# Kernel tuning notes

Hardware: AMD Instinct MI355X
Metric: run time of the kernel (lower is better)

Reference implementation:

```python
import jax, jax.numpy as jnp
import numpy as np

# --- HashGrid constants (from init_kwargs) ---
L = 16                 # num_lods
T = 1 << 18            # hashmap entries per level (codebook_bitwidth=18)
F = 2                  # feature_dim per level
BASE = 16              # min_width_codebook
MAXW = 1 << 12         # max_width_codebook
SCALE = np.exp((np.log(MAXW) - np.log(BASE)) / L)
RES = np.floor(BASE * SCALE ** np.arange(L)).astype(np.float32)  # per-level grid resolution
P1 = np.uint32(2654435761)  # coherent-prime hash primes (prime for x is 1)
P2 = np.uint32(805459861)
OFFS = np.array([[i, j, k] for i in (0, 1) for j in (0, 1) for k in (0, 1)], np.int32)  # [8,3] cube corners


def _hash_encode(x, tables):
    """x: [N,3] in [0,1]. tables: [L,T,F]. Returns [N, 3 + L*F] (include_xyz)."""
    def level(table, res):
        xs = x * res                              # [N,3] scaled coords
        x0 = jnp.floor(xs)
        t = xs - x0                               # fractional part
        w = t * t * (3.0 - 2.0 * t)               # Smoothstep interpolation weights
        c = x0.astype(jnp.int32)[:, None, :] + OFFS[None]    # [N,8,3] corner coords
        cu = c.astype(jnp.uint32)
        h = (cu[..., 0] ^ (cu[..., 1] * P1) ^ (cu[..., 2] * P2)) & jnp.uint32(T - 1)  # [N,8]
        feats = table[h]                          # [N,8,F] irregular gather
        wts = jnp.prod(jnp.where(OFFS[None] == 1, w[:, None, :], 1.0 - w[:, None, :]), axis=-1)  # [N,8]
        return jnp.einsum('ncf,nc->nf', feats, wts)  # [N,F]

    f = jax.vmap(level)(tables, jnp.asarray(RES))   # [L,N,F]
    f = jnp.moveaxis(f, 0, 1).reshape(x.shape[0], L * F)
    return jnp.concatenate([x, f], axis=-1)         # include_xyz prepends raw coords


def setup_inputs() -> dict:
    key = jax.random.key(0)
    k1, k2, k3, k4 = jax.random.split(key, 4)
    N = 1 << 20
    x = jax.random.uniform(k1, (N, 3), dtype=jnp.float32)
    tables = jax.random.normal(k2, (L, T, F), dtype=jnp.float32) * 1e-2
    d_in = 3 + L * F    # 35
    W1 = jax.random.normal(k3, (d_in, 128), dtype=jnp.float32) / np.sqrt(d_in)
    W2 = jax.random.normal(k4, (128, 129), dtype=jnp.float32) / np.sqrt(128.0)
    return {"x": x, "tables": tables, "W1": W1, "W2": W2}


def reference(x, tables, W1, W2):
    enc = _hash_encode(x, tables)        # [N,35]
    h = jax.nn.relu(enc @ W1)            # VanillaMLP: one hidden layer, bias-free
    return h @ W2                        # [N, 1+geo_feat_dim], Identity output act
```

## Files before the change

### kernel.cpp

```cpp
#include <hip/hip_runtime.h>

typedef __attribute__((ext_vector_type(8))) short short8;
typedef __attribute__((ext_vector_type(4))) float f32x4;
typedef __attribute__((ext_vector_type(4))) int int4v;

#define TMASK  ((1u << 18) - 1u)
#define PRIME1 2654435761u
#define PRIME2 805459861u

__constant__ float c_res[16] = {16.f, 22.f, 31.f, 45.f, 63.f, 90.f, 127.f, 181.f,
                                255.f, 362.f, 511.f, 724.f, 1023.f, 1448.f, 2047.f, 2896.f};

__device__ __forceinline__ unsigned short rne_bf16(float v) {
  unsigned u = __builtin_bit_cast(unsigned, v);
  return (unsigned short)((u + 0x7fffu + ((u >> 16) & 1u)) >> 16);
}
__device__ __forceinline__ float b2f(unsigned short h) {
  unsigned u = (unsigned)h << 16;
  return __builtin_bit_cast(float, u);
}

__device__ __forceinline__ float2 enc_level(float x0, float x1, float x2, int lvl,
                                            const float* __restrict__ Tb) {
  const float r = c_res[lvl];
  const float xs0 = x0 * r, xs1 = x1 * r, xs2 = x2 * r;
  const float f0 = floorf(xs0), f1 = floorf(xs1), f2 = floorf(xs2);
  const float t0 = xs0 - f0, t1 = xs1 - f1, t2 = xs2 - f2;
  const float w0 = t0 * t0 * (3.f - 2.f * t0);
  const float w1v = t1 * t1 * (3.f - 2.f * t1);
  const float w2v = t2 * t2 * (3.f - 2.f * t2);
  const unsigned cx0 = (unsigned)(int)f0;
  const unsigned hy0 = (unsigned)(int)f1 * PRIME1, hy1 = hy0 + PRIME1;
  const unsigned hz0 = (unsigned)(int)f2 * PRIME2, hz1 = hz0 + PRIME2;
  const float2* tab = reinterpret_cast<const float2*>(Tb) + ((size_t)lvl << 18);
  float a0 = 0.f, a1 = 0.f;
  if (!(cx0 & 1u)) {
    const float4* tab4 = reinterpret_cast<const float4*>(tab);
#pragma unroll
    for (int jk = 0; jk < 4; ++jk) {
      const unsigned hb = (cx0 ^ ((jk & 2) ? hy1 : hy0) ^ ((jk & 1) ? hz1 : hz0)) & TMASK;
      const float4 q = tab4[hb >> 1];
      float e0x, e0y, e1x, e1y;
      if (hb & 1) { e0x = q.z; e0y = q.w; e1x = q.x; e1y = q.y; }
      else        { e0x = q.x; e0y = q.y; e1x = q.z; e1y = q.w; }
      const float wy = (jk & 2) ? w1v : 1.f - w1v;
      const float wz = (jk & 1) ? w2v : 1.f - w2v;
      const float wt0 = ((1.f - w0) * wy) * wz;
      const float wt1 = (w0 * wy) * wz;
      a0 = fmaf(e0x, wt0, a0); a1 = fmaf(e0y, wt0, a1);
      a0 = fmaf(e1x, wt1, a0); a1 = fmaf(e1y, wt1, a1);
    }
  } else {
#pragma unroll
    for (int c = 0; c < 8; ++c) {
      const unsigned hx = cx0 + (unsigned)((c >> 2) & 1);
      const unsigned hh = (hx ^ ((c & 2) ? hy1 : hy0) ^ ((c & 1) ? hz1 : hz0)) & TMASK;
      const float2 f = tab[hh];
      const float wt = (((c >> 2) & 1) ? w0 : 1.f - w0) *
                       (((c >> 1) & 1) ? w1v : 1.f - w1v) *
                       (((c & 1)) ? w2v : 1.f - w2v);
      a0 = fmaf(f.x, wt, a0);
      a1 = fmaf(f.y, wt, a1);
    }
  }
  return make_float2(a0, a1);
}

__global__ __launch_bounds__(256, 2) void fused_pc(
    const float* __restrict__ X, const float* __restrict__ Tb,
    const float* __restrict__ W1, const float* __restrict__ W2,
    unsigned short* __restrict__ encF, int* __restrict__ flags,
    float* __restrict__ Out) {
  __shared__ __align__(16) unsigned char lds[76800];
  __shared__ int ldsflag;
  unsigned short* w1S  = (unsigned short*)lds;
  float*          w1x  = (float*)(lds + 8192);
  float*          xyzS = (float*)(lds + 9728);
  unsigned short* w2hS = (unsigned short*)(lds + 10752);
  float*          hS   = (float*)(lds + 43776);
  float*          outS = (float*)(lds + 43776);

  const int tid = threadIdx.x;
  const int lane = tid & 63, w = tid >> 6;
  const int b = blockIdx.x;
  const int g = b & 7;
  const int bslot = b >> 3;
  const int lvlA = g, lvlB = 15 - g;

  for (int idx = tid; idx < 32 * 128; idx += 256) {
    const int k = idx >> 7, col = idx & 127;
    w1S[((k >> 3) * 128 + col) * 8 + (k & 7)] = rne_bf16(W1[(k + 3) * 128 + col]);
  }
  for (int idx = tid; idx < 3 * 128; idx += 256) w1x[idx] = W1[idx];
  for (int idx = tid; idx < 128 * 129; idx += 256) {
    const int k = idx / 129, col = idx - k * 129;
    w2hS[((k >> 3) * 129 + col) * 8 + (k & 7)] = rne_bf16(W2[idx]);
  }
  __syncthreads();

  int nextI = 0;

  auto mlp_chunk = [&](int chunk) {
    const size_t base_int = ((size_t)(chunk * 4 + w) * 64 + lane) * 4;
    int4v ai;
#pragma unroll
    for (int e = 0; e < 4; ++e)
      ai[e] = __hip_atomic_load((int*)encF + base_int + e,
                                __ATOMIC_RELAXED, __HIP_MEMORY_SCOPE_SYSTEM);
    const short8 af = __builtin_bit_cast(short8, ai);
    const int row0 = chunk << 6;
    if (tid < 192) xyzS[(tid / 3) * 4 + (tid % 3)] = X[(size_t)row0 * 3 + tid];
    __syncthreads();

    f32x4 acc1[8];
#pragma unroll
    for (int c = 0; c < 8; ++c) acc1[c] = (f32x4){0.f, 0.f, 0.f, 0.f};
#pragma unroll
    for (int c = 0; c < 8; ++c) {
      const short8 bb = *reinterpret_cast<const short8*>(
          &w1S[((lane >> 4) * 128 + c * 16 + (lane & 15)) * 8]);
      acc1[c] = __builtin_amdgcn_mfma_f32_16x16x32_bf16(af, bb, acc1[c], 0, 0, 0);
    }
#pragma unroll
    for (int r = 0; r < 4; ++r) {
      const int grow = (w << 4) + (lane >> 4) * 4 + r;
      const float xs0 = xyzS[grow * 4 + 0];
      const float xs1 = xyzS[grow * 4 + 1];
      const float xs2 = xyzS[grow * 4 + 2];
#pragma unroll
      for (int c = 0; c < 8; ++c) {
        const int col = c * 16 + (lane & 15);
        float v = acc1[c][r];
        v = fmaf(xs0, w1x[col], v);
        v = fmaf(xs1, w1x[128 + col], v);
        v = fmaf(xs2, w1x[256 + col], v);
        acc1[c][r] = v;
      }
    }
#pragma unroll
    for (int c = 0; c < 8; ++c) {
#pragma unroll
      for (int r = 0; r < 4; ++r) {
        const int row = (w << 4) + (lane >> 4) * 4 + r;
        const int col = c * 16 + (lane & 15);
        const int cc = (col >> 2) ^ (row & 7);
        hS[row * 128 + (cc << 2) + (col & 3)] = fmaxf(acc1[c][r], 0.f);
      }
    }
    __syncthreads();

    const int arow = (w << 4) + (lane & 15);
    short8 a2h[4], a2l[4];
#pragma unroll
    for (int kc = 0; kc < 4; ++kc) {
      const int c8 = kc * 4 + (lane >> 4);
      const int base = arow * 128;
      const int cc0 = (2 * c8) ^ (arow & 7);
      const int cc1 = (2 * c8 + 1) ^ (arow & 7);
      const f32x4 q0 = *reinterpret_cast<const f32x4*>(&hS[base + (cc0 << 2)]);
      const f32x4 q1 = *reinterpret_cast<const f32x4*>(&hS[base + (cc1 << 2)]);
#pragma unroll
      for (int e = 0; e < 4; ++e) {
        const unsigned short hi = rne_bf16(q0[e]);
        a2h[kc][e] = (short)hi;
        a2l[kc][e] = (short)rne_bf16(q0[e] - b2f(hi));
      }
#pragma unroll
      for (int e = 0; e < 4; ++e) {
        const unsigned short hi = rne_bf16(q1[e]);
        a2h[kc][4 + e] = (short)hi;
        a2l[kc][4 + e] = (short)rne_bf16(q1[e] - b2f(hi));
      }
    }
    __syncthreads();

#pragma unroll
    for (int c = 0; c < 9; ++c) {
      f32x4 acc = (f32x4){0.f, 0.f, 0.f, 0.f};
      int bcol = c * 16 + (lane & 15);
      if (bcol > 128) bcol = 128;
#pragma unroll
      for (int kc = 0; kc < 4; ++kc) {
        const int c8 = kc * 4 + (lane >> 4);
        const short8 bh = *reinterpret_cast<const short8*>(&w2hS[(c8 * 129 + bcol) * 8]);
        acc = __builtin_amdgcn_mfma_f32_16x16x32_bf16(a2h[kc], bh, acc, 0, 0, 0);
        acc = __builtin_amdgcn_mfma_f32_16x16x32_bf16(a2l[kc], bh, acc, 0, 0, 0);
      }
      const int col = c * 16 + (lane & 15);
      if (col < 129) {
#pragma unroll
        for (int r = 0; r < 4; ++r) {
          const int lrow = (w << 4) + (lane >> 4) * 4 + r;
          outS[lrow * 129 + col] = acc[r];
        }
      }
    }
    __syncthreads();

    float* dst = Out + (size_t)row0 * 129;
    const f32x4* src = (const f32x4*)outS;
    for (int i = tid; i < 2064; i += 256)
      __builtin_nontemporal_store(src[i], reinterpret_cast<f32x4*>(dst + 4 * i));
  };

  for (int t = 0; t < 64; ++t) {
    const int grp = bslot + t * 64;
    {
      const int p = (grp << 8) + tid;
      const float x0 = X[p * 3 + 0];
      const float x1 = X[p * 3 + 1];
      const float x2 = X[p * 3 + 2];
      const int pl = p & 63, chunk = p >> 6;
      const size_t rowbase = ((size_t)(chunk * 4 + (pl >> 4)) * 64 + (pl & 15)) * 8;
#pragma unroll
      for (int li = 0; li < 2; ++li) {
        const int lvl = li ? lvlB : lvlA;
        const float2 a = enc_level(x0, x1, x2, lvl, Tb);
        const int c8 = lvl >> 2;
        const size_t addr_short = rowbase + (size_t)(c8 << 7) + (lvl & 3) * 2;
        const int val = (int)rne_bf16(a.x) | ((int)rne_bf16(a.y) << 16);
        __hip_atomic_store((int*)encF + (addr_short >> 1), val,
                           __ATOMIC_RELAXED, __HIP_MEMORY_SCOPE_SYSTEM);
      }
    }
    __syncthreads();
    if (tid == 0)
      __hip_atomic_fetch_add(&flags[grp], 1, __ATOMIC_RELAXED, __HIP_MEMORY_SCOPE_SYSTEM);

    while (nextI < 32) {
      const int c = b + (nextI << 9);
      if (tid == 0)
        ldsflag = __hip_atomic_load(&flags[c >> 2], __ATOMIC_RELAXED,
                                    __HIP_MEMORY_SCOPE_SYSTEM);
      __syncthreads();
      if (ldsflag != 8) break;
      mlp_chunk(c);
      ++nextI;
    }
  }

  while (nextI < 32) {
    const int c = b + (nextI << 9);
    for (;;) {
      if (tid == 0)
        ldsflag = __hip_atomic_load(&flags[c >> 2], __ATOMIC_RELAXED,
                                    __HIP_MEMORY_SCOPE_SYSTEM);
      __syncthreads();
      if (ldsflag == 8) break;
      __builtin_amdgcn_s_sleep(32);
      __syncthreads();
    }
    mlp_chunk(c);
    ++nextI;
  }
}

__global__ __launch_bounds__(256) void fused_hashmlp(
    const float* __restrict__ X, const float* __restrict__ Tb,
    const float* __restrict__ W1, const float* __restrict__ W2,
    float* __restrict__ Out, int nChunks) {
  __shared__ __align__(16) unsigned char lds[147968];
  unsigned short* w1hS = (unsigned short*)lds;
  unsigned short* w1lS = w1hS + 128 * 64;
  unsigned short* w2hS = (unsigned short*)(lds + 32768);
  unsigned short* w2lS = w2hS + 129 * 128;
  unsigned short* enchS = (unsigned short*)(lds + 98816);
  unsigned short* enclS = enchS + 64 * 64;
  float*          hS    = (float*)(lds + 115200);
  float*          outS  = (float*)(lds + 98816);

  const int tid = threadIdx.x;
  for (int idx = tid; idx < 128 * 64; idx += 256) {
    int k = idx >> 7, col = idx & 127;
    float v = 0.f;
    if (k < 35) { int r = (k < 32) ? (k + 3) : (k - 32); v = W1[r * 128 + col]; }
    unsigned short hi = rne_bf16(v);
    unsigned short lo = rne_bf16(v - b2f(hi));
    int a = col * 64 + (k ^ ((col & 7) << 3));
    w1hS[a] = hi; w1lS[a] = lo;
  }
  for (int idx = tid; idx < 129 * 128; idx += 256) {
    int k = idx / 129, col = idx - k * 129;
    float v = W2[k * 129 + col];
    unsigned short hi = rne_bf16(v);
    unsigned short lo = rne_bf16(v - b2f(hi));
    int a = col * 128 + (k ^ ((col & 7) << 3));
    w2hS[a] = hi; w2lS[a] = lo;
  }
  __syncthreads();

  const int p = tid >> 2, s = tid & 3, lane = tid & 63, w = tid >> 6;
  for (int chunk = blockIdx.x; chunk < nChunks; chunk += gridDim.x) {
    const int row0 = chunk * 64;
    {
      const int gp = row0 + p;
      const float x0 = X[gp * 3 + 0], x1 = X[gp * 3 + 1], x2 = X[gp * 3 + 2];
      short8 pkh, pkl;
#pragma unroll
      for (int li = 0; li < 4; ++li) {
        const int lvl = (s << 2) + li;
        const float2 a = enc_level(x0, x1, x2, lvl, Tb);
        unsigned short h0 = rne_bf16(a.x), h1 = rne_bf16(a.y);
        pkh[li * 2 + 0] = (short)h0; pkh[li * 2 + 1] = (short)h1;
        pkl[li * 2 + 0] = (short)rne_bf16(a.x - b2f(h0));
        pkl[li * 2 + 1] = (short)rne_bf16(a.y - b2f(h1));
      }
      const int coff = (s ^ (p & 7)) << 3;
      *reinterpret_cast<short8*>(&enchS[p * 64 + coff]) = pkh;
      *reinterpret_cast<short8*>(&enclS[p * 64 + coff]) = pkl;
      short8 zh, zl;
#pragma unroll
      for (int e = 0; e < 8; ++e) { zh[e] = 0; zl[e] = 0; }
      if (s == 0) {
        unsigned short hx0 = rne_bf16(x0), hx1 = rne_bf16(x1), hx2 = rne_bf16(x2);
        zh[0] = (short)hx0; zh[1] = (short)hx1; zh[2] = (short)hx2;
        zl[0] = (short)rne_bf16(x0 - b2f(hx0));
        zl[1] = (short)rne_bf16(x1 - b2f(hx1));
        zl[2] = (short)rne_bf16(x2 - b2f(hx2));
      }
      const int coff2 = ((4 + s) ^ (p & 7)) << 3;
      *reinterpret_cast<short8*>(&enchS[p * 64 + coff2]) = zh;
      *reinterpret_cast<short8*>(&enclS[p * 64 + coff2]) = zl;
    }
    __syncthreads();
    f32x4 acc1[8];
#pragma unroll
    for (int c = 0; c < 8; ++c) acc1[c] = (f32x4){0.f, 0.f, 0.f, 0.f};
    {
      const int arow = (w << 4) + (lane & 15);
#pragma unroll
      for (int kc = 0; kc < 2; ++kc) {
        const int c8 = kc * 4 + (lane >> 4);
        const int aoff = arow * 64 + ((c8 ^ (arow & 7)) << 3);
        const short8 ah = *reinterpret_cast<const short8*>(&enchS[aoff]);
        const short8 al = *reinterpret_cast<const short8*>(&enclS[aoff]);
#pragma unroll
        for (int c = 0; c < 8; ++c) {
          const int bcol = c * 16 + (lane & 15);
          const int boff = bcol * 64 + ((c8 ^ (bcol & 7)) << 3);
          const short8 bh = *reinterpret_cast<const short8*>(&w1hS[boff]);
          const short8 bl = *reinterpret_cast<const short8*>(&w1lS[boff]);
          acc1[c] = __builtin_amdgcn_mfma_f32_16x16x32_bf16(ah, bh, acc1[c], 0, 0, 0);
          acc1[c] = __builtin_amdgcn_mfma_f32_16x16x32_bf16(ah, bl, acc1[c], 0, 0, 0);
          acc1[c] = __builtin_amdgcn_mfma_f32_16x16x32_bf16(al, bh, acc1[c], 0, 0, 0);
        }
      }
    }
#pragma unroll
    for (int c = 0; c < 8; ++c) {
#pragma unroll
      for (int r = 0; r < 4; ++r) {
        const int row = (w << 4) + (lane >> 4) * 4 + r;
        const int col = c * 16 + (lane & 15);
        const int cc = (col >> 2) ^ (row & 7);
        hS[row * 128 + (cc << 2) + (col & 3)] = fmaxf(acc1[c][r], 0.f);
      }
    }
    __syncthreads();
    {
      const int arow = (w << 4) + (lane & 15);
      short8 a2h[4], a2l[4];
#pragma unroll
      for (int kc = 0; kc < 4; ++kc) {
        const int c8 = kc * 4 + (lane >> 4);
        const int base = arow * 128;
        const int cc0 = (2 * c8) ^ (arow & 7);
        const int cc1 = (2 * c8 + 1) ^ (arow & 7);
        const f32x4 q0 = *reinterpret_cast<const f32x4*>(&hS[base + (cc0 << 2)]);
        const f32x4 q1 = *reinterpret_cast<const f32x4*>(&hS[base + (cc1 << 2)]);
#pragma unroll
        for (int e = 0; e < 4; ++e) {
          unsigned short hi = rne_bf16(q0[e]);
          a2h[kc][e] = (short)hi;
          a2l[kc][e] = (short)rne_bf16(q0[e] - b2f(hi));
        }
#pragma unroll
        for (int e = 0; e < 4; ++e) {
          unsigned short hi = rne_bf16(q1[e]);
          a2h[kc][4 + e] = (short)hi;
          a2l[kc][4 + e] = (short)rne_bf16(q1[e] - b2f(hi));
        }
      }
      __syncthreads();
#pragma unroll
      for (int c = 0; c < 9; ++c) {
        f32x4 acc = (f32x4){0.f, 0.f, 0.f, 0.f};
        int bcol = c * 16 + (lane & 15);
        if (bcol > 128) bcol = 128;
#pragma unroll
        for (int kc = 0; kc < 4; ++kc) {
          const int c8 = kc * 4 + (lane >> 4);
          const int boff = bcol * 128 + ((c8 ^ (bcol & 7)) << 3);
          const short8 bh = *reinterpret_cast<const short8*>(&w2hS[boff]);
          const short8 bl = *reinterpret_cast<const short8*>(&w2lS[boff]);
          acc = __builtin_amdgcn_mfma_f32_16x16x32_bf16(a2h[kc], bh, acc, 0, 0, 0);
          acc = __builtin_amdgcn_mfma_f32_16x16x32_bf16(a2h[kc], bl, acc, 0, 0, 0);
          acc = __builtin_amdgcn_mfma_f32_16x16x32_bf16(a2l[kc], bh, acc, 0, 0, 0);
        }
        const int col = c * 16 + (lane & 15);
        if (col < 129) {
#pragma unroll
          for (int r = 0; r < 4; ++r) {
            const int lrow = (w << 4) + (lane >> 4) * 4 + r;
            outS[lrow * 129 + col] = acc[r];
          }
        }
      }
    }
    __syncthreads();
    {
      float* dst = Out + (size_t)row0 * 129;
      const f32x4* src = (const f32x4*)outS;
      for (int i = tid; i < 2064; i += 256)
        *reinterpret_cast<f32x4*>(dst + 4 * i) = src[i];
    }
    __syncthreads();
  }
}

extern "C" void kernel_launch(void* const* d_in, const int* in_sizes, int n_in,
                              void* d_out, int out_size, void* d_ws, size_t ws_size,
                              hipStream_t stream) {
  const float* X  = (const float*)d_in[0];
  const float* Tb = (const float*)d_in[1];
  const float* W1 = (const float*)d_in[2];
  const float* W2 = (const float*)d_in[3];
  float* Out = (float*)d_out;

  const int N = in_sizes[0] / 3;
  const int nChunks = N / 64;

  const size_t encBytes = (size_t)nChunks * 4096;
  const size_t flagBytes = 4096 * sizeof(int);
  if (N == (1 << 20) && ws_size >= encBytes + flagBytes) {
    unsigned short* encF = (unsigned short*)d_ws;
    int* flags = (int*)((char*)d_ws + encBytes);
    hipMemsetAsync(flags, 0, flagBytes, stream);
    fused_pc<<<512, 256, 0, stream>>>(X, Tb, W1, W2, encF, flags, Out);
  } else {
    int grid = nChunks < 1024 ? nChunks : 1024;
    fused_hashmlp<<<grid, 256, 0, stream>>>(X, Tb, W1, W2, Out, nChunks);
  }
}
```

Measured before the change: 642.6 us.

## Pack both levels' bf16 features into one 64-bit store per point

Changes the intermediate encoding buffer layout so each point's two levels (lvlA, lvlB) are packed into a single 8-byte cell, written with one atomic 64-bit store instead of two scattered 32-bit stores. The W1 shared-memory layout is permuted to match the new K ordering, and the MLP side reads two coalesced 64-bit atomic loads per lane instead of four 32-bit loads. This targets the cost of scattered fine-grained atomic stores and loads through the producer/consumer buffer. It depends on the W1 row permutation exactly matching the packed level order.

New measurement: 625.4 us. 1.03x faster.

```diff
diff --git a/kernel.cpp b/kernel.cpp
--- a/kernel.cpp
+++ b/kernel.cpp
@@ -2,7 +2,7 @@
 
 typedef __attribute__((ext_vector_type(8))) short short8;
 typedef __attribute__((ext_vector_type(4))) float f32x4;
-typedef __attribute__((ext_vector_type(4))) int int4v;
+typedef __attribute__((ext_vector_type(2))) unsigned long long u64x2;
 
 #define TMASK  ((1u << 18) - 1u)
 #define PRIME1 2654435761u
@@ -89,7 +89,11 @@
 
   for (int idx = tid; idx < 32 * 128; idx += 256) {
     const int k = idx >> 7, col = idx & 127;
-    w1S[((k >> 3) * 128 + col) * 8 + (k & 7)] = rne_bf16(W1[(k + 3) * 128 + col]);
+    const int s = k >> 3, j = k & 7;
+    const int lvl = (j < 2) ? 2 * s : (j < 4) ? (15 - 2 * s)
+                  : (j < 6) ? (2 * s + 1) : (14 - 2 * s);
+    const int row = 3 + 2 * lvl + (j & 1);
+    w1S[(s * 128 + col) * 8 + j] = rne_bf16(W1[row * 128 + col]);
   }
   for (int idx = tid; idx < 3 * 128; idx += 256) w1x[idx] = W1[idx];
   for (int idx = tid; idx < 128 * 129; idx += 256) {
@@ -101,13 +105,16 @@
   int nextI = 0;
 
   auto mlp_chunk = [&](int chunk) {
-    const size_t base_int = ((size_t)(chunk * 4 + w) * 64 + lane) * 4;
-    int4v ai;
-#pragma unroll
-    for (int e = 0; e < 4; ++e)
-      ai[e] = __hip_atomic_load((int*)encF + base_int + e,
-                                __ATOMIC_RELAXED, __HIP_MEMORY_SCOPE_SYSTEM);
-    const short8 af = __builtin_bit_cast(short8, ai);
+    const int s = lane >> 4;
+    const int pl = (w << 4) | (lane & 15);
+    const unsigned long long* e8 =
+        (const unsigned long long*)encF + (size_t)chunk * 512 + pl;
+    u64x2 av;
+    av[0] = __hip_atomic_load(e8 + (size_t)(2 * s) * 64,
+                              __ATOMIC_RELAXED, __HIP_MEMORY_SCOPE_SYSTEM);
+    av[1] = __hip_atomic_load(e8 + (size_t)(2 * s + 1) * 64,
+                              __ATOMIC_RELAXED, __HIP_MEMORY_SCOPE_SYSTEM);
+    const short8 af = __builtin_bit_cast(short8, av);
     const int row0 = chunk << 6;
     if (tid < 192) xyzS[(tid / 3) * 4 + (tid % 3)] = X[(size_t)row0 * 3 + tid];
     __syncthreads();
@@ -118,7 +125,7 @@
 #pragma unroll
     for (int c = 0; c < 8; ++c) {
       const short8 bb = *reinterpret_cast<const short8*>(
-          &w1S[((lane >> 4) * 128 + c * 16 + (lane & 15)) * 8]);
+          &w1S[(s * 128 + c * 16 + (lane & 15)) * 8]);
       acc1[c] = __builtin_amdgcn_mfma_f32_16x16x32_bf16(af, bb, acc1[c], 0, 0, 0);
     }
 #pragma unroll
@@ -210,18 +217,17 @@
       const float x0 = X[p * 3 + 0];
       const float x1 = X[p * 3 + 1];
       const float x2 = X[p * 3 + 2];
+      const float2 aA = enc_level(x0, x1, x2, lvlA, Tb);
+      const float2 aB = enc_level(x0, x1, x2, lvlB, Tb);
+      const unsigned long long cell =
+          (unsigned long long)rne_bf16(aA.x)
+          | ((unsigned long long)rne_bf16(aA.y) << 16)
+          | ((unsigned long long)rne_bf16(aB.x) << 32)
+          | ((unsigned long long)rne_bf16(aB.y) << 48);
       const int pl = p & 63, chunk = p >> 6;
-      const size_t rowbase = ((size_t)(chunk * 4 + (pl >> 4)) * 64 + (pl & 15)) * 8;
-#pragma unroll
-      for (int li = 0; li < 2; ++li) {
-        const int lvl = li ? lvlB : lvlA;
-        const float2 a = enc_level(x0, x1, x2, lvl, Tb);
-        const int c8 = lvl >> 2;
-        const size_t addr_short = rowbase + (size_t)(c8 << 7) + (lvl & 3) * 2;
-        const int val = (int)rne_bf16(a.x) | ((int)rne_bf16(a.y) << 16);
-        __hip_atomic_store((int*)encF + (addr_short >> 1), val,
-                           __ATOMIC_RELAXED, __HIP_MEMORY_SCOPE_SYSTEM);
-      }
+      __hip_atomic_store((unsigned long long*)encF
+                             + (size_t)chunk * 512 + (size_t)g * 64 + pl,
+                         cell, __ATOMIC_RELAXED, __HIP_MEMORY_SCOPE_SYSTEM);
     }
     __syncthreads();
     if (tid == 0)
```
